# Performance work log

Hardware: AMD Instinct MI355X
Metric: run time of the kernel (lower is better)

Reference implementation:

```python
import jax, jax.numpy as jnp
import numpy as np

N = 50000          # nodes
DEG = 16           # graph_max_neighbor
E = N * DEG        # edges (sorted by receiver)
DIM = 128          # config.hidden_dimension
EDGE_DIM = 32
EPS = 1e-5


def _ln(x, scale, offset, mask):
    # masked LayerNorm over last axis: normalize per row, then apply node mask
    m = jnp.mean(x, axis=-1, keepdims=True)
    v = jnp.mean(jnp.square(x - m), axis=-1, keepdims=True)
    return ((x - m) * jax.lax.rsqrt(v + EPS) * scale + offset) * mask


def setup_inputs() -> dict:
    key = jax.random.key(0)
    ks = jax.random.split(key, 12)
    node_inp = jax.random.normal(ks[0], (N, DIM), jnp.float32)
    edge_feat = jax.random.normal(ks[1], (E, EDGE_DIM), jnp.float32)
    node_mask = jnp.ones((N, 1), jnp.float32)
    senders = jax.random.randint(ks[2], (E,), 0, N, jnp.int32)
    receivers = jnp.repeat(jnp.arange(N, dtype=jnp.int32), DEG)  # sorted, DEG per node
    din_e = 2 * DIM + EDGE_DIM
    s = lambda d: 1.0 / np.sqrt(d)
    We1 = jax.random.normal(ks[3], (din_e, 2 * DIM), jnp.float32) * s(din_e)
    be1 = jnp.zeros((2 * DIM,), jnp.float32)
    We2 = jax.random.normal(ks[4], (2 * DIM, DIM), jnp.float32) * s(2 * DIM)
    be2 = jnp.zeros((DIM,), jnp.float32)
    g_msg = jnp.ones((DIM,), jnp.float32)
    b_msg = jnp.zeros((DIM,), jnp.float32)
    Wn1 = jax.random.normal(ks[5], (2 * DIM, 2 * DIM), jnp.float32) * s(2 * DIM)
    bn1 = jnp.zeros((2 * DIM,), jnp.float32)
    Wn2 = jax.random.normal(ks[6], (2 * DIM, DIM), jnp.float32) * s(2 * DIM)
    bn2 = jnp.zeros((DIM,), jnp.float32)
    g_node = jnp.ones((DIM,), jnp.float32)
    b_node = jnp.zeros((DIM,), jnp.float32)
    return dict(node_inp=node_inp, edge_feat=edge_feat, node_mask=node_mask,
                We1=We1, be1=be1, We2=We2, be2=be2, g_msg=g_msg, b_msg=b_msg,
                Wn1=Wn1, bn1=bn1, Wn2=Wn2, bn2=bn2, g_node=g_node, b_node=b_node,
                senders=senders, receivers=receivers)


def reference(node_inp, edge_feat, node_mask, We1, be1, We2, be2, g_msg, b_msg,
              Wn1, bn1, Wn2, bn2, g_node, b_node, senders, receivers):
    # gather + concat -> edge MLP (swish, no final activation; haiku MLP default)
    msg_input = jnp.concatenate(
        [node_inp[senders], node_inp[receivers], edge_feat], axis=-1)  # [E, 2*DIM+EDGE_DIM]
    h = jax.nn.swish(msg_input @ We1 + be1)
    messages = h @ We2 + be2                                           # [E, DIM]
    # scatter-reduce to receivers (sorted), mean over max neighbors
    agg = jax.ops.segment_sum(messages, receivers, num_segments=node_inp.shape[0],
                              indices_are_sorted=True) / DEG
    agg = _ln(agg, g_msg, b_msg, node_mask)
    # node update MLP + residual + masked LN
    nf = jnp.concatenate([node_inp, agg], axis=-1)                     # [N, 2*DIM]
    nf = jax.nn.swish(nf @ Wn1 + bn1) @ Wn2 + bn2                      # [N, DIM]
    nf = node_inp + nf
    return _ln(nf, g_node, b_node, node_mask)
```

## Files before the change

kernel.cpp:

```cpp
#include <hip/hip_runtime.h>

typedef _Float16 F16;
typedef _Float16 half8 __attribute__((ext_vector_type(8)));
typedef _Float16 half2 __attribute__((ext_vector_type(2)));
typedef float f32x4 __attribute__((ext_vector_type(4)));

#define N_NODES 50000
#define DEG 16
#define N_EDGES (N_NODES * DEG)
#define DIM 128

#define NEG_LOG2E -1.442695041f
#define MEAN_UNSCALE -0.04332169878f

__device__ __forceinline__ float frcp(float x) { float r; asm("v_rcp_f32 %0, %1" : "=v"(r) : "v"(x)); return r; }
__device__ __forceinline__ float frsq(float x) { float r; asm("v_rsq_f32 %0, %1" : "=v"(r) : "v"(x)); return r; }
__device__ __forceinline__ float fexp2(float x) { float r; asm("v_exp_f32 %0, %1" : "=v"(r) : "v"(x)); return r; }
__device__ __forceinline__ float swishf(float x) { return x * frcp(1.0f + fexp2(x * NEG_LOG2E)); }

__device__ __forceinline__ half8 cvt8(f32x4 a, f32x4 b) {
    half8 h; h[0]=(F16)a[0]; h[1]=(F16)a[1]; h[2]=(F16)a[2]; h[3]=(F16)a[3];
    h[4]=(F16)b[0]; h[5]=(F16)b[1]; h[6]=(F16)b[2]; h[7]=(F16)b[3]; return h;
}

__device__ __forceinline__ void pack_one(const float* src, F16* dst, int idx,
                                         int K, int NC, int ld, int row0, int split,
                                         float scale) {
    int j = idx & 7;
    int l = (idx >> 3) & 63;
    int blob = idx >> 9;
    int ntiles = NC >> 4;
    int tcol = blob % ntiles;
    int c = blob / ntiles;
    int k = c * 32 + ((l >> 4) * 8) + j;
    int col = tcol * 16 + (l & 15);
    int sr = row0 + k, sc = col;
    if (split && col >= split) { sr += K; sc -= split; }
    dst[idx] = (F16)(src[(size_t)sr * ld + sc] * scale);
}

__global__ void k_pack_all(const float* __restrict__ We1, const float* __restrict__ We2,
                           const float* __restrict__ Wn1, const float* __restrict__ Wn2,
                           F16* w1abp, F16* w1ep, F16* we2p, F16* wn1p, F16* wn2p) {
    int b = blockIdx.x, t = threadIdx.x;
    if (b < 256)      pack_one(We1, w1abp, (b - 0)   * 256 + t, 128, 512, 256, 0,   256, NEG_LOG2E);
    else if (b < 288) pack_one(We1, w1ep,  (b - 256) * 256 + t, 32,  256, 256, 256, 0,   NEG_LOG2E);
    else if (b < 416) pack_one(We2, we2p,  (b - 288) * 256 + t, 256, 128, 128, 0,   0,   1.0f);
    else if (b < 672) pack_one(Wn1, wn1p,  (b - 416) * 256 + t, 256, 256, 256, 0,   0,   1.0f);
    else              pack_one(Wn2, wn2p,  (b - 672) * 256 + t, 256, 128, 128, 0,   0,   1.0f);
}

#define PAS 152
__global__ __launch_bounds__(256, 2) void k_proj(
    const float* __restrict__ node_inp, const float* __restrict__ be1,
    const F16* __restrict__ w1abp, F16* __restrict__ Ps, F16* __restrict__ Pr)
{
    __shared__ __align__(16) F16 A[64 * PAS];
    const int t = threadIdx.x;
    const int n0 = blockIdx.x * 64;

    #pragma unroll
    for (int i = 0; i < 4; ++i) {
        int id = t + i * 256; int row = id >> 4, c = id & 15;
        int gn = n0 + row; if (gn >= N_NODES) gn = N_NODES - 1;
        f32x4 v0 = *(const f32x4*)(node_inp + (size_t)gn * DIM + c * 8);
        f32x4 v1 = *(const f32x4*)(node_inp + (size_t)gn * DIM + c * 8 + 4);
        *(half8*)&A[row * PAS + c * 8] = cvt8(v0, v1);
    }
    __syncthreads();

    const int lane = t & 63, wn = t >> 6;
    const int lcol = lane & 15, quad = lane >> 4;

    f32x4 acc[4][8] = {};
    #pragma unroll
    for (int c = 0; c < 4; ++c) {
        half8 af[4];
        #pragma unroll
        for (int rt = 0; rt < 4; ++rt)
            af[rt] = *(const half8*)&A[(rt * 16 + lcol) * PAS + c * 32 + quad * 8];
        const F16* wp = w1abp + (((size_t)(c * 32 + wn * 8)) * 64 + lane) * 8;
        #pragma unroll
        for (int nt = 0; nt < 8; ++nt) {
            half8 bv = *(const half8*)(wp + (size_t)nt * 512);
            #pragma unroll
            for (int rt = 0; rt < 4; ++rt)
                acc[rt][nt] = __builtin_amdgcn_mfma_f32_16x16x32_f16(af[rt], bv, acc[rt][nt], 0, 0, 0);
        }
    }

    F16* dst = (wn < 2) ? Ps : Pr;
    const int cb = (wn & 1) * 128;
    #pragma unroll
    for (int nt = 0; nt < 8; ++nt) {
        int col = cb + nt * 16 + lcol;
        float bias = (wn >= 2) ? be1[col] * NEG_LOG2E : 0.0f;
        #pragma unroll
        for (int rt = 0; rt < 4; ++rt) {
            #pragma unroll
            for (int r = 0; r < 4; ++r) {
                int gn = n0 + rt * 16 + quad * 4 + r;
                if (gn < N_NODES) dst[(size_t)gn * 256 + col] = (F16)(acc[rt][nt][r] + bias);
            }
        }
    }
}

#define PGS2 136
__global__ __launch_bounds__(256, 5) void k_edge(
    const F16* __restrict__ Ps, const F16* Pr,
    const float* __restrict__ edge_feat, const int* __restrict__ senders,
    const F16* __restrict__ w1ep, F16* Hm)
{
    __shared__ __align__(16) F16 Pg[4 * 16 * PGS2];
    __shared__ __align__(16) F16 Hs[4][128];
    const int t = threadIdx.x;
    const int n0 = blockIdx.x * 4;
    const int e0 = n0 * 16;
    const int lane = t & 63, nd = t >> 6;
    const int lcol = lane & 15, quad = lane >> 4;
    const int n = n0 + nd;

    int srow[4];
    #pragma unroll
    for (int i = 0; i < 4; ++i) srow[i] = senders[e0 + nd * 16 + quad + i * 4];

    const float* efp = edge_feat + (size_t)(e0 + nd * 16 + lcol) * 32 + quad * 8;
    f32x4 v0 = __builtin_nontemporal_load((const f32x4*)efp);
    f32x4 v1 = __builtin_nontemporal_load((const f32x4*)(efp + 4));

    half8 prv[2], psv[2][4];
    #pragma unroll
    for (int h = 0; h < 2; ++h) {
        prv[h] = *(const half8*)(Pr + (size_t)n * 256 + h * 128 + lcol * 8);
        #pragma unroll
        for (int i = 0; i < 4; ++i)
            psv[h][i] = *(const half8*)(Ps + (size_t)srow[i] * 256 + h * 128 + lcol * 8);
    }
    half8 a = cvt8(v0, v1);

    F16* pg = &Pg[nd * 16 * PGS2];
    #pragma unroll
    for (int h = 0; h < 2; ++h) {
        #pragma unroll
        for (int i = 0; i < 4; ++i)
            *(half8*)&pg[(quad + i * 4) * PGS2 + lcol * 8] = psv[h][i] + prv[h];

        f32x4 acc[8] = {};
        #pragma unroll
        for (int j = 0; j < 8; ++j) {
            half8 bv = *(const half8*)(w1ep + (((size_t)(h * 8 + j)) * 64 + lane) * 8);
            acc[j] = __builtin_amdgcn_mfma_f32_16x16x32_f16(a, bv, acc[j], 0, 0, 0);
        }
        F16 hv8[8];
        #pragma unroll
        for (int j = 0; j < 8; ++j) {
            const F16* pgp = &pg[(quad * 4) * PGS2 + j * 16 + lcol];
            float s = 0.f;
            #pragma unroll
            for (int r = 0; r < 4; ++r) {
                float x = acc[j][r] + (float)pgp[r * PGS2];
                s = __builtin_fmaf(x, frcp(1.0f + fexp2(x)), s);
            }
            s += __shfl_xor(s, 16, 64);
            s += __shfl_xor(s, 32, 64);
            hv8[j] = (F16)(s * MEAN_UNSCALE);
        }
        if (lane < 16) {
            #pragma unroll
            for (int j = 0; j < 8; ++j) Hs[nd][j * 16 + lane] = hv8[j];
            half8 hrow = *(const half8*)&Hs[nd][lane * 8];
            *(half8*)(Hm + (size_t)n * 256 + h * 128 + lane * 8) = hrow;
        }
    }
}

#define XS 280
#define FSS 139
__global__ __launch_bounds__(256, 4) void k_node(
    const float* __restrict__ node_inp, const F16* Hm,
    const float* __restrict__ be2, const float* __restrict__ g_msg, const float* __restrict__ b_msg,
    const float* __restrict__ bn1, const float* __restrict__ bn2,
    const float* __restrict__ g_node, const float* __restrict__ b_node,
    const float* __restrict__ node_mask,
    const F16* __restrict__ we2p, const F16* __restrict__ wn1p, const F16* __restrict__ wn2p,
    float* out)
{
    __shared__ __align__(16) unsigned char smem[64 * XS * 2];
    F16* X = (F16*)smem;
    float* Fs = (float*)smem;

    const int t = threadIdx.x;
    const int n0 = blockIdx.x * 64;
    const int lane = t & 63, w = t >> 6;
    const int lcol = lane & 15, quad = lane >> 4;

    #pragma unroll
    for (int i = 0; i < 4; ++i) {
        int id = t + i * 256; int row = id >> 4, c = id & 15;
        int gn = n0 + row; if (gn >= N_NODES) gn = N_NODES - 1;
        f32x4 v0 = *(const f32x4*)(node_inp + (size_t)gn * DIM + c * 8);
        f32x4 v1 = *(const f32x4*)(node_inp + (size_t)gn * DIM + c * 8 + 4);
        *(half8*)&X[row * XS + c * 8] = cvt8(v0, v1);
    }

    {
        const int r0 = w * 16;
        int gr = n0 + r0 + lcol; if (gr >= N_NODES) gr = N_NODES - 1;
        const F16* hrow = Hm + (size_t)gr * 256;
        f32x4 acc[8] = {};
        #pragma unroll
        for (int c = 0; c < 8; ++c) {
            half8 af = *(const half8*)(hrow + c * 32 + quad * 8);
            const F16* wp = we2p + (((size_t)(c * 8)) * 64 + lane) * 8;
            #pragma unroll
            for (int nt = 0; nt < 8; ++nt) {
                half8 bv = *(const half8*)(wp + (size_t)nt * 512);
                acc[nt] = __builtin_amdgcn_mfma_f32_16x16x32_f16(af, bv, acc[nt], 0, 0, 0);
            }
        }
        #pragma unroll
        for (int nt = 0; nt < 8; ++nt) {
            int col = nt * 16 + lcol;
            float b = be2[col];
            #pragma unroll
            for (int r = 0; r < 4; ++r)
                X[(r0 + quad * 4 + r) * XS + 128 + col] = (F16)(acc[nt][r] + b);
        }
    }
    __syncthreads();

    {
        int row = t >> 2, q = t & 3;
        int gn = n0 + row; if (gn >= N_NODES) gn = N_NODES - 1;
        float vv[32]; float sum = 0.f, sq = 0.f;
        #pragma unroll
        for (int j = 0; j < 4; ++j) {
            half8 hv = *(const half8*)&X[row * XS + 128 + q * 32 + j * 8];
            #pragma unroll
            for (int k = 0; k < 8; ++k) { float f = (float)hv[k]; vv[j*8+k] = f; sum += f; sq += f*f; }
        }
        sum += __shfl_xor(sum, 1, 64); sq += __shfl_xor(sq, 1, 64);
        sum += __shfl_xor(sum, 2, 64); sq += __shfl_xor(sq, 2, 64);
        float mean = sum * (1.0f / DIM);
        float rs = frsq(sq * (1.0f / DIM) - mean * mean + 1e-5f);
        float msk = node_mask[gn];
        #pragma unroll
        for (int j = 0; j < 16; ++j) {
            int col = q * 32 + j * 2;
            half2 o;
            o[0] = (F16)(((vv[j*2]   - mean) * rs * g_msg[col]   + b_msg[col])   * msk);
            o[1] = (F16)(((vv[j*2+1] - mean) * rs * g_msg[col+1] + b_msg[col+1]) * msk);
            *(half2*)&X[row * XS + 128 + col] = o;
        }
    }
    __syncthreads();

    {
        f32x4 acc1[4][4] = {};
        #pragma unroll
        for (int c = 0; c < 8; ++c) {
            half8 af[4];
            #pragma unroll
            for (int rt = 0; rt < 4; ++rt)
                af[rt] = *(const half8*)&X[(rt * 16 + lcol) * XS + c * 32 + quad * 8];
            const F16* wp = wn1p + (((size_t)(c * 16 + w * 4)) * 64 + lane) * 8;
            #pragma unroll
            for (int nt = 0; nt < 4; ++nt) {
                half8 bv = *(const half8*)(wp + (size_t)nt * 512);
                #pragma unroll
                for (int rt = 0; rt < 4; ++rt)
                    acc1[rt][nt] = __builtin_amdgcn_mfma_f32_16x16x32_f16(af[rt], bv, acc1[rt][nt], 0, 0, 0);
            }
        }
        __syncthreads();
        #pragma unroll
        for (int nt = 0; nt < 4; ++nt) {
            int col = w * 64 + nt * 16 + lcol;
            float b = bn1[col];
            #pragma unroll
            for (int rt = 0; rt < 4; ++rt)
                #pragma unroll
                for (int r = 0; r < 4; ++r) {
                    float x = acc1[rt][nt][r] + b;
                    X[(rt * 16 + quad * 4 + r) * XS + col] = (F16)swishf(x);
                }
        }
    }
    __syncthreads();

    {
        f32x4 acc2[4][2] = {};
        #pragma unroll
        for (int c = 0; c < 8; ++c) {
            half8 af[4];
            #pragma unroll
            for (int rt = 0; rt < 4; ++rt)
                af[rt] = *(const half8*)&X[(rt * 16 + lcol) * XS + c * 32 + quad * 8];
            const F16* wp = wn2p + (((size_t)(c * 8 + w * 2)) * 64 + lane) * 8;
            #pragma unroll
            for (int nt = 0; nt < 2; ++nt) {
                half8 bv = *(const half8*)(wp + (size_t)nt * 512);
                #pragma unroll
                for (int rt = 0; rt < 4; ++rt)
                    acc2[rt][nt] = __builtin_amdgcn_mfma_f32_16x16x32_f16(af[rt], bv, acc2[rt][nt], 0, 0, 0);
            }
        }
        __syncthreads();
        #pragma unroll
        for (int nt = 0; nt < 2; ++nt) {
            int col = w * 32 + nt * 16 + lcol;
            float b = bn2[col];
            #pragma unroll
            for (int rt = 0; rt < 4; ++rt)
                #pragma unroll
                for (int r = 0; r < 4; ++r)
                    Fs[(rt * 16 + quad * 4 + r) * FSS + col] = acc2[rt][nt][r] + b;
        }
    }
    __syncthreads();

    {
        int row = t >> 2, q = t & 3;
        int gn = n0 + row;
        f32x4 xr[8];
        float sum = 0.f, sq = 0.f;
        if (gn < N_NODES) {
            #pragma unroll
            for (int j = 0; j < 8; ++j) {
                f32x4 aa = *(const f32x4*)&Fs[row * FSS + q * 32 + j * 4];
                f32x4 ni = *(const f32x4*)(node_inp + (size_t)gn * DIM + q * 32 + j * 4);
                f32x4 x = aa + ni;
                xr[j] = x;
                sum += x[0] + x[1] + x[2] + x[3];
                sq  += x[0]*x[0] + x[1]*x[1] + x[2]*x[2] + x[3]*x[3];
            }
        }
        sum += __shfl_xor(sum, 1, 64); sq += __shfl_xor(sq, 1, 64);
        sum += __shfl_xor(sum, 2, 64); sq += __shfl_xor(sq, 2, 64);
        if (gn < N_NODES) {
            float mean = sum * (1.0f / DIM);
            float rs = frsq(sq * (1.0f / DIM) - mean * mean + 1e-5f);
            float msk = node_mask[gn];
            #pragma unroll
            for (int j = 0; j < 8; ++j) {
                f32x4 o;
                #pragma unroll
                for (int qq = 0; qq < 4; ++qq) {
                    int col = q * 32 + j * 4 + qq;
                    o[qq] = ((xr[j][qq] - mean) * rs * g_node[col] + b_node[col]) * msk;
                }
                *(f32x4*)(out + (size_t)gn * DIM + q * 32 + j * 4) = o;
            }
        }
    }
}


extern "C" void kernel_launch(void* const* d_in, const int* in_sizes, int n_in,
                              void* d_out, int out_size, void* d_ws, size_t ws_size,
                              hipStream_t stream)
{
    const float* node_inp  = (const float*)d_in[0];
    const float* edge_feat = (const float*)d_in[1];
    const float* node_mask = (const float*)d_in[2];
    const float* We1 = (const float*)d_in[3];
    const float* be1 = (const float*)d_in[4];
    const float* We2 = (const float*)d_in[5];
    const float* be2 = (const float*)d_in[6];
    const float* g_msg = (const float*)d_in[7];
    const float* b_msg = (const float*)d_in[8];
    const float* Wn1 = (const float*)d_in[9];
    const float* bn1 = (const float*)d_in[10];
    const float* Wn2 = (const float*)d_in[11];
    const float* bn2 = (const float*)d_in[12];
    const float* g_node = (const float*)d_in[13];
    const float* b_node = (const float*)d_in[14];
    const int* senders = (const int*)d_in[15];
    float* out = (float*)d_out;

    char* ws = (char*)d_ws;
    F16* Ps = (F16*)ws;
    size_t off = (size_t)N_NODES * 256 * 2;
    F16* w1abp = (F16*)(ws + off); off += 128 * 512 * 2;
    F16* w1ep  = (F16*)(ws + off); off += 32 * 256 * 2;
    F16* we2p  = (F16*)(ws + off); off += 256 * 128 * 2;
    F16* wn1p  = (F16*)(ws + off); off += 256 * 256 * 2;
    F16* wn2p  = (F16*)(ws + off); off += 256 * 128 * 2;

    F16* PrHm = (F16*)d_out;

    k_pack_all<<<dim3(800), dim3(256), 0, stream>>>(We1, We2, Wn1, Wn2,
                                                    w1abp, w1ep, we2p, wn1p, wn2p);

    k_proj<<<dim3((N_NODES + 63) / 64), dim3(256), 0, stream>>>(node_inp, be1, w1abp, Ps, PrHm);

    k_edge<<<dim3(N_NODES / 4), dim3(256), 0, stream>>>(Ps, PrHm, edge_feat, senders, w1ep, PrHm);

    k_node<<<dim3((N_NODES + 63) / 64), dim3(256), 0, stream>>>(
        node_inp, PrHm, be2, g_msg, b_msg, bn1, bn2, g_node, b_node, node_mask,
        we2p, wn1p, wn2p, out);
}
```

Measured before the change: 338.2 us.

## Reduce edge swish sums via MFMA with ones; split proj into two passes

In the edge kernel, the per-column reduction over 16 edges, previously done with two cross-lane shuffles, is replaced by a 16x16x16 f16 MFMA against a ones vector, with the swish values rounded to fp16 before summing. The projection kernel processes its 256 output columns in two passes of 4 accumulator tiles instead of 8, halving accumulator registers so it can run with launch bounds of 4 blocks. The edge kernel's launch-bound occupancy is lowered from 5 to 4. Summing in fp16 inputs adds rounding error and relies on the builtin being available.

```diff
diff --git a/kernel.cpp b/kernel.cpp
--- a/kernel.cpp
+++ b/kernel.cpp
@@ -2,6 +2,7 @@
 
 typedef _Float16 F16;
 typedef _Float16 half8 __attribute__((ext_vector_type(8)));
+typedef _Float16 half4 __attribute__((ext_vector_type(4)));
 typedef _Float16 half2 __attribute__((ext_vector_type(2)));
 typedef float f32x4 __attribute__((ext_vector_type(4)));
 
@@ -51,7 +52,7 @@
 }
 
 #define PAS 152
-__global__ __launch_bounds__(256, 2) void k_proj(
+__global__ __launch_bounds__(256, 4) void k_proj(
     const float* __restrict__ node_inp, const float* __restrict__ be1,
     const F16* __restrict__ w1abp, F16* __restrict__ Ps, F16* __restrict__ Pr)
 {
@@ -72,42 +73,44 @@
     const int lane = t & 63, wn = t >> 6;
     const int lcol = lane & 15, quad = lane >> 4;
 
-    f32x4 acc[4][8] = {};
-    #pragma unroll
-    for (int c = 0; c < 4; ++c) {
-        half8 af[4];
-        #pragma unroll
-        for (int rt = 0; rt < 4; ++rt)
-            af[rt] = *(const half8*)&A[(rt * 16 + lcol) * PAS + c * 32 + quad * 8];
-        const F16* wp = w1abp + (((size_t)(c * 32 + wn * 8)) * 64 + lane) * 8;
-        #pragma unroll
-        for (int nt = 0; nt < 8; ++nt) {
-            half8 bv = *(const half8*)(wp + (size_t)nt * 512);
+    #pragma unroll
+    for (int p = 0; p < 2; ++p) {
+        f32x4 acc[4][4] = {};
+        #pragma unroll
+        for (int c = 0; c < 4; ++c) {
+            half8 af[4];
             #pragma unroll
             for (int rt = 0; rt < 4; ++rt)
-                acc[rt][nt] = __builtin_amdgcn_mfma_f32_16x16x32_f16(af[rt], bv, acc[rt][nt], 0, 0, 0);
-        }
-    }
-
-    F16* dst = (wn < 2) ? Ps : Pr;
-    const int cb = (wn & 1) * 128;
-    #pragma unroll
-    for (int nt = 0; nt < 8; ++nt) {
-        int col = cb + nt * 16 + lcol;
-        float bias = (wn >= 2) ? be1[col] * NEG_LOG2E : 0.0f;
-        #pragma unroll
-        for (int rt = 0; rt < 4; ++rt) {
-            #pragma unroll
-            for (int r = 0; r < 4; ++r) {
-                int gn = n0 + rt * 16 + quad * 4 + r;
-                if (gn < N_NODES) dst[(size_t)gn * 256 + col] = (F16)(acc[rt][nt][r] + bias);
+                af[rt] = *(const half8*)&A[(rt * 16 + lcol) * PAS + c * 32 + quad * 8];
+            const F16* wp = w1abp + (((size_t)(c * 32 + p * 16 + wn * 4)) * 64 + lane) * 8;
+            #pragma unroll
+            for (int nt = 0; nt < 4; ++nt) {
+                half8 bv = *(const half8*)(wp + (size_t)nt * 512);
+                #pragma unroll
+                for (int rt = 0; rt < 4; ++rt)
+                    acc[rt][nt] = __builtin_amdgcn_mfma_f32_16x16x32_f16(af[rt], bv, acc[rt][nt], 0, 0, 0);
+            }
+        }
+
+        F16* dst = p ? Pr : Ps;
+        #pragma unroll
+        for (int nt = 0; nt < 4; ++nt) {
+            int col = wn * 64 + nt * 16 + lcol;
+            float bias = p ? be1[col] * NEG_LOG2E : 0.0f;
+            #pragma unroll
+            for (int rt = 0; rt < 4; ++rt) {
+                #pragma unroll
+                for (int r = 0; r < 4; ++r) {
+                    int gn = n0 + rt * 16 + quad * 4 + r;
+                    if (gn < N_NODES) dst[(size_t)gn * 256 + col] = (F16)(acc[rt][nt][r] + bias);
+                }
             }
         }
     }
 }
 
 #define PGS2 136
-__global__ __launch_bounds__(256, 5) void k_edge(
+__global__ __launch_bounds__(256, 4) void k_edge(
     const F16* __restrict__ Ps, const F16* Pr,
     const float* __restrict__ edge_feat, const int* __restrict__ senders,
     const F16* __restrict__ w1ep, F16* Hm)
@@ -152,7 +155,22 @@
             half8 bv = *(const half8*)(w1ep + (((size_t)(h * 8 + j)) * 64 + lane) * 8);
             acc[j] = __builtin_amdgcn_mfma_f32_16x16x32_f16(a, bv, acc[j], 0, 0, 0);
         }
-        F16 hv8[8];
+
+#if __has_builtin(__builtin_amdgcn_mfma_f32_16x16x16f16)
+        const half4 ones4 = {(F16)1.0f, (F16)1.0f, (F16)1.0f, (F16)1.0f};
+        #pragma unroll
+        for (int j = 0; j < 8; ++j) {
+            const F16* pgp = &pg[(quad * 4) * PGS2 + j * 16 + lcol];
+            half4 wv;
+            #pragma unroll
+            for (int r = 0; r < 4; ++r) {
+                float x = acc[j][r] + (float)pgp[r * PGS2];
+                wv[r] = (F16)(x * frcp(1.0f + fexp2(x)));
+            }
+            f32x4 cs = __builtin_amdgcn_mfma_f32_16x16x16f16(ones4, wv, (f32x4){0.f,0.f,0.f,0.f}, 0, 0, 0);
+            if (lane < 16) Hs[nd][j * 16 + lane] = (F16)(cs[0] * MEAN_UNSCALE);
+        }
+#else
         #pragma unroll
         for (int j = 0; j < 8; ++j) {
             const F16* pgp = &pg[(quad * 4) * PGS2 + j * 16 + lcol];
@@ -164,11 +182,10 @@
             }
             s += __shfl_xor(s, 16, 64);
             s += __shfl_xor(s, 32, 64);
-            hv8[j] = (F16)(s * MEAN_UNSCALE);
-        }
+            if (lane < 16) Hs[nd][j * 16 + lane] = (F16)(s * MEAN_UNSCALE);
+        }
+#endif
         if (lane < 16) {
-            #pragma unroll
-            for (int j = 0; j < 8; ++j) Hs[nd][j * 16 + lane] = hv8[j];
             half8 hrow = *(const half8*)&Hs[nd][lane * 8];
             *(half8*)(Hm + (size_t)n * 256 + h * 128 + lane * 8) = hrow;
         }
```

Result: slower. 380.6 us (+12.5%).
